# Performance work log

Measured on AMD Instinct MI355X. Metric: run time of the kernel, lower is better.

Reference implementation:

```python
import jax, jax.numpy as jnp
import numpy as np

B, C, H, W = 2, 192, 128, 128
NUM_HEADS = 6
AMP = 1
NUM_OFFSETS = 9


def bilinear_sample(img, grid):
    # img: (C, H, W); grid: (Hn, Wn, 2) in [-1,1], align_corners=True, zeros padding
    Hh, Ww = img.shape[1], img.shape[2]
    x = (grid[..., 0] + 1.0) * 0.5 * (Ww - 1)
    y = (grid[..., 1] + 1.0) * 0.5 * (Hh - 1)
    x0 = jnp.floor(x)
    y0 = jnp.floor(y)
    x1 = x0 + 1.0
    y1 = y0 + 1.0
    wx1 = x - x0
    wy1 = y - y0

    def gather(yi, xi):
        valid = ((xi >= 0) & (xi <= Ww - 1) & (yi >= 0) & (yi <= Hh - 1)).astype(img.dtype)
        xc = jnp.clip(xi, 0, Ww - 1).astype(jnp.int32)
        yc = jnp.clip(yi, 0, Hh - 1).astype(jnp.int32)
        return img[:, yc, xc] * valid  # (C, Hn, Wn)

    return (gather(y0, x0) * ((1 - wy1) * (1 - wx1))
            + gather(y0, x1) * ((1 - wy1) * wx1)
            + gather(y1, x0) * (wy1 * (1 - wx1))
            + gather(y1, x1) * (wy1 * wx1))


def setup_inputs() -> dict:
    key = jax.random.key(0)
    ks = jax.random.split(key, 8)
    s = 0.02
    Ch = C // NUM_HEADS
    return {
        "x_q": jax.random.normal(ks[0], (B, C, H, W), jnp.float32),
        "x_kv": jax.random.normal(ks[1], (B, C, H, W), jnp.float32),
        "w_q": jax.random.normal(ks[2], (C, C), jnp.float32) * s,
        "w_kv": jax.random.normal(ks[3], (2 * C, C), jnp.float32) * s,
        "w_off1": jax.random.normal(ks[4], (C, 2 * C, 3, 3), jnp.float32) * s,
        "b_off1": jnp.zeros((C,), jnp.float32),
        "w_off2": jax.random.normal(ks[5], (2 * NUM_OFFSETS, C), jnp.float32) * s,
        "b_off2": jnp.zeros((2 * NUM_OFFSETS,), jnp.float32),
        "w_proj": jax.random.normal(ks[6], (C, C), jnp.float32) * s,
        "b_proj": jnp.zeros((C,), jnp.float32),
    }


def reference(x_q, x_kv, w_q, w_kv, w_off1, b_off1, w_off2, b_off2, w_proj, b_proj):
    Ch = C // NUM_HEADS
    scale = Ch ** (-0.5)

    # 1x1 conv projections as channel matmuls
    q = jnp.einsum('oc,bchw->bohw', w_q, x_q) * scale
    kv = jnp.einsum('oc,bchw->bohw', w_kv, x_kv)
    k, v = kv[:, :C], kv[:, C:]  # kv.reshape(B,2,Ch,nh,H,W) -> first C channels are k

    # offset predictor: 3x3 conv -> relu -> 1x1 conv
    off_in = jnp.concatenate([x_q, x_kv], axis=1)
    h1 = jax.lax.conv_general_dilated(off_in, w_off1, (1, 1), 'SAME',
                                      dimension_numbers=('NCHW', 'OIHW', 'NCHW'))
    h1 = jax.nn.relu(h1 + b_off1[None, :, None, None])
    off = jnp.einsum('oc,bchw->bohw', w_off2, h1) + b_off2[None, :, None, None]
    off = off.reshape(B, NUM_OFFSETS, 2, H, W).transpose(0, 1, 3, 4, 2)  # (B,9,H,W,2)
    gx = off[..., 0] / (W - 1) * 2.0 - 1.0
    gy = off[..., 1] / (H - 1) * 2.0 - 1.0
    grid = jnp.stack([gx, gy], axis=-1)  # (B,9,H,W,2)

    # deformable gather: sample full-channel k/v at each of 9 per-pixel offset grids
    sample = jax.vmap(jax.vmap(bilinear_sample, in_axes=(None, 0)), in_axes=(0, 0))
    k_s = sample(k, grid).reshape(B, NUM_OFFSETS, Ch, NUM_HEADS, H, W)
    v_s = sample(v, grid).reshape(B, NUM_OFFSETS, Ch, NUM_HEADS, H, W)

    q = q.reshape(B, Ch, NUM_HEADS, H, W)

    pad = [(0, 0), (0, 0), (0, 0), (0, 0), (AMP, AMP), (AMP, AMP)]
    k_p = jnp.pad(k_s, pad)
    v_p = jnp.pad(v_s, pad)

    win = 2 * AMP + 1
    logits = []
    for i in range(win):
        for j in range(win):
            idx = i * win + j
            kp = k_p[:, idx, :, :, i:i + H, j:j + W]  # (B,Ch,nh,H,W)
            logits.append(jnp.einsum('bchxy,bchxy->bhxy', q, kp))
    attn = jax.nn.softmax(jnp.stack(logits, axis=1), axis=1)  # (B,9,nh,H,W)

    out = jnp.zeros((B, Ch, NUM_HEADS, H, W), x_q.dtype)
    for i in range(win):
        for j in range(win):
            idx = i * win + j
            vp = v_p[:, idx, :, :, i:i + H, j:j + W]
            out = out + attn[:, idx, None] * vp

    out = out.reshape(B, C, H, W)  # channel layout = (Ch, nh), matching torch reshape
    return jnp.einsum('oc,bchw->bohw', w_proj, out) + b_proj[None, :, None, None]
```

## Files before the change

### kernel.cpp

```cpp
#include <hip/hip_runtime.h>
#include <math.h>

#define HW 16384
#define NB 2
#define NC 192

typedef __attribute__((ext_vector_type(8))) short bh8;
typedef __attribute__((ext_vector_type(4))) float f32x4;

__device__ inline ushort f2bf(float f) {
  union { float f; unsigned int u; } x; x.f = f;
  unsigned int r = x.u + 0x7fffu + ((x.u >> 16) & 1u);
  return (ushort)(r >> 16);
}
__device__ inline float bf2f(ushort u) {
  union { unsigned int i; float f; } x; x.i = ((unsigned int)u) << 16;
  return x.f;
}
__device__ inline float asf(unsigned int u) {
  union { unsigned int i; float f; } x; x.i = u; return x.f;
}
__device__ inline unsigned int cvtpk(float lo, float hi) {
  unsigned int r;
  asm("v_cvt_pk_bf16_f32 %0, %1, %2" : "=v"(r) : "v"(lo), "v"(hi));
  return r;
}
__device__ inline void gl16(const ushort* g, char* l) {
  __builtin_amdgcn_global_load_lds(
      (const __attribute__((address_space(1))) unsigned int*)g,
      (__attribute__((address_space(3))) unsigned int*)l, 16, 0, 0);
}

__global__ void k_wpack(const float* __restrict__ w1, ushort* __restrict__ wpack) {
  int i = blockIdx.x * 256 + threadIdx.x;
  int s = i / 6144;
  int rem = i - s * 6144;
  int o = rem >> 5, kk = rem & 31;
  int dy = s / 36, t2 = s - dy * 36;
  int icc = t2 / 3, dxi = t2 - icc * 3;
  int ic = icc * 32 + kk;
  wpack[i] = f2bf(w1[(size_t)o * 3456 + (size_t)ic * 9 + dy * 3 + dxi]);
}

__global__ void k_wgpack(const float* __restrict__ wq, const float* __restrict__ wkv,
                         const float* __restrict__ wp, float scale,
                         ushort* __restrict__ wg) {
  int i = blockIdx.x * 256 + threadIdx.x;
  int r = i / NC, c = i - r * NC;
  float v;
  if (r < 192) {
    int orow = (r & 31) * 6 + (r >> 5);
    v = wq[(size_t)orow * NC + c] * scale;
  } else if (r < 576) {
    int rp = r - 192;
    int t = rp >= 192 ? 1 : 0;
    int cc = rp - t * 192;
    int orow = t * 192 + (cc & 31) * 6 + (cc >> 5);
    v = wkv[(size_t)orow * NC + c];
  } else {
    int rp = r - 576;
    v = wp[(size_t)rp * NC + ((c & 31) * 6 + (c >> 5))];
  }
  wg[i] = f2bf(v);
}

__global__ void k_zero(uint4* __restrict__ p) {
  p[(size_t)blockIdx.x * 256 + threadIdx.x] = make_uint4(0u, 0u, 0u, 0u);
}

__global__ __launch_bounds__(256) void k_xpack(const float* __restrict__ xq,
                                               const float* __restrict__ xkv,
                                               ushort* __restrict__ xpp) {
  __shared__ float t[NC][65];
  const int tid = threadIdx.x;
  const size_t r0 = (size_t)blockIdx.x * 64;
  const int b = (int)(r0 >> 14);
  const int px0 = (int)(r0 & 16383);
  const int y = px0 >> 7, x0 = px0 & 127;
  const float* src = (blockIdx.y == 0 ? xq : xkv) + (size_t)b * NC * HW + px0;
#pragma unroll
  for (int it = 0; it < 12; ++it) {
    int i = it * 256 + tid;
    int c = i >> 4, q4 = i & 15;
    float4 v = *(const float4*)(src + (size_t)c * HW + q4 * 4);
    t[c][q4 * 4 + 0] = v.x; t[c][q4 * 4 + 1] = v.y;
    t[c][q4 * 4 + 2] = v.z; t[c][q4 * 4 + 3] = v.w;
  }
  __syncthreads();
  ushort* dst = xpp + ((size_t)(b * 130 + y + 1) * 132 + x0 + 1) * 384 +
                blockIdx.y * 192;
#pragma unroll
  for (int it = 0; it < 6; ++it) {
    int i = it * 256 + tid;
    int px = i / 24, ch = i - px * 24;
    ushort4 u0, u1;
    u0.x = f2bf(t[ch * 8 + 0][px]); u0.y = f2bf(t[ch * 8 + 1][px]);
    u0.z = f2bf(t[ch * 8 + 2][px]); u0.w = f2bf(t[ch * 8 + 3][px]);
    u1.x = f2bf(t[ch * 8 + 4][px]); u1.y = f2bf(t[ch * 8 + 5][px]);
    u1.z = f2bf(t[ch * 8 + 6][px]); u1.w = f2bf(t[ch * 8 + 7][px]);
    *(ushort4*)&dst[(size_t)px * 384 + ch * 8] = u0;
    *(ushort4*)&dst[(size_t)px * 384 + ch * 8 + 4] = u1;
  }
}

__device__ inline void stage64(ushort* lds, const ushort* src, int rowStride,
                               int tid) {
#pragma unroll
  for (int it = 0; it < 6; ++it) {
    int i = it * 256 + tid;
    int row = i / 24, c = i - row * 24;
    int pos = (c & 24) | ((c & 7) ^ (row & 7));
    uint4 v = *(const uint4*)(src + (size_t)row * rowStride + c * 8);
    *(uint4*)&lds[row * NC + pos * 8] = v;
  }
}
__device__ inline bh8 frag64(const ushort* lds, int row, int c) {
  int pos = (c & 24) | ((c & 7) ^ (row & 7));
  return *(const bh8*)&lds[row * NC + pos * 8];
}

__global__ __launch_bounds__(256) void k_gemm_mfma(
    const ushort* __restrict__ xpp, const ushort* __restrict__ wg,
    ushort* __restrict__ qb, ushort* __restrict__ kb, ushort* __restrict__ vb) {
  __shared__ __attribute__((aligned(16))) ushort xs[64 * NC];
  __shared__ __attribute__((aligned(16))) ushort ws2[64 * NC];
  const int tid = threadIdx.x;
  const size_t p0 = (size_t)blockIdx.x * 64;
  const int bb = (int)(p0 >> 14);
  const int yy = (int)((p0 >> 7) & 127);
  const int xx0 = (int)(p0 & 127);
  const int which = blockIdx.y;
  const int cOff = (which == 0) ? 0 : 192;
  const ushort* src = xpp + ((size_t)(bb * 130 + yy + 1) * 132 + xx0 + 1) * 384 + cOff;
  const ushort* wbase = wg + (size_t)(which * 192) * NC;
  ushort* dst = which == 0 ? qb : (which == 1 ? kb : vb);
  stage64(xs, src, 384, tid);
  const int lid = tid & 15, g = (tid >> 4) & 3, wv = tid >> 6;
  const int wo = (wv & 1) * 32, wp = (wv >> 1) * 32;
  for (int ot = 0; ot < 3; ++ot) {
    if (ot) __syncthreads();
    stage64(ws2, wbase + (size_t)(ot * 64) * NC, NC, tid);
    __syncthreads();
    f32x4 acc[2][2];
#pragma unroll
    for (int m = 0; m < 2; ++m)
#pragma unroll
      for (int n = 0; n < 2; ++n) acc[m][n] = (f32x4){0.f, 0.f, 0.f, 0.f};
#pragma unroll
    for (int k = 0; k < 6; ++k) {
      bh8 a0 = frag64(ws2, wo + lid, k * 4 + g);
      bh8 a1 = frag64(ws2, wo + 16 + lid, k * 4 + g);
      bh8 b0 = frag64(xs, wp + lid, k * 4 + g);
      bh8 b1 = frag64(xs, wp + 16 + lid, k * 4 + g);
      acc[0][0] = __builtin_amdgcn_mfma_f32_16x16x32_bf16(a0, b0, acc[0][0], 0, 0, 0);
      acc[0][1] = __builtin_amdgcn_mfma_f32_16x16x32_bf16(a0, b1, acc[0][1], 0, 0, 0);
      acc[1][0] = __builtin_amdgcn_mfma_f32_16x16x32_bf16(a1, b0, acc[1][0], 0, 0, 0);
      acc[1][1] = __builtin_amdgcn_mfma_f32_16x16x32_bf16(a1, b1, acc[1][1], 0, 0, 0);
    }
    const int od = ot * 64;
#pragma unroll
    for (int m = 0; m < 2; ++m)
#pragma unroll
      for (int n = 0; n < 2; ++n) {
        int orow = od + wo + m * 16 + g * 4;
        size_t px = p0 + wp + n * 16 + lid;
        ushort4 u;
        u.x = f2bf(acc[m][n][0]); u.y = f2bf(acc[m][n][1]);
        u.z = f2bf(acc[m][n][2]); u.w = f2bf(acc[m][n][3]);
        *(ushort4*)&dst[px * NC + orow] = u;
      }
  }
}

__global__ __launch_bounds__(256) void k_proj_mfma(
    const ushort* __restrict__ pre, const ushort* __restrict__ wg,
    const float* __restrict__ bp, float* __restrict__ out) {
  __shared__ __attribute__((aligned(16))) ushort xs[64 * NC];
  __shared__ __attribute__((aligned(16))) ushort ws2[64 * NC];
  const int tid = threadIdx.x;
  const size_t p0 = (size_t)blockIdx.x * 64;
  const int o0 = blockIdx.y * 64;
  stage64(xs, pre + p0 * NC, NC, tid);
  stage64(ws2, wg + (size_t)o0 * NC, NC, tid);
  __syncthreads();
  const int lid = tid & 15, g = (tid >> 4) & 3, wv = tid >> 6;
  const int wo = (wv & 1) * 32, wp = (wv >> 1) * 32;
  f32x4 acc[2][2];
#pragma unroll
  for (int m = 0; m < 2; ++m)
#pragma unroll
    for (int n = 0; n < 2; ++n) acc[m][n] = (f32x4){0.f, 0.f, 0.f, 0.f};
#pragma unroll
  for (int k = 0; k < 6; ++k) {
    bh8 a0 = frag64(ws2, wo + lid, k * 4 + g);
    bh8 a1 = frag64(ws2, wo + 16 + lid, k * 4 + g);
    bh8 b0 = frag64(xs, wp + lid, k * 4 + g);
    bh8 b1 = frag64(xs, wp + 16 + lid, k * 4 + g);
    acc[0][0] = __builtin_amdgcn_mfma_f32_16x16x32_bf16(a0, b0, acc[0][0], 0, 0, 0);
    acc[0][1] = __builtin_amdgcn_mfma_f32_16x16x32_bf16(a0, b1, acc[0][1], 0, 0, 0);
    acc[1][0] = __builtin_amdgcn_mfma_f32_16x16x32_bf16(a1, b0, acc[1][0], 0, 0, 0);
    acc[1][1] = __builtin_amdgcn_mfma_f32_16x16x32_bf16(a1, b1, acc[1][1], 0, 0, 0);
  }
#pragma unroll
  for (int m = 0; m < 2; ++m)
#pragma unroll
    for (int n = 0; n < 2; ++n) {
      int oc = o0 + wo + m * 16 + g * 4;
      size_t pxf = p0 + wp + n * 16 + lid;
      int b = (int)(pxf >> 14);
      int px = (int)(pxf & 16383);
#pragma unroll
      for (int j = 0; j < 4; ++j)
        out[((size_t)b * NC + oc + j) * HW + px] = acc[m][n][j] + bp[oc + j];
    }
}

#define CP0 0
#define CP1 8448
#define CW0 16896
#define CW1 35328
__global__ __launch_bounds__(256, 3) void k_conv_mfma(
    const ushort* __restrict__ xpp, const ushort* __restrict__ wpack,
    const float* __restrict__ b1, ushort* __restrict__ h1) {
  __shared__ __attribute__((aligned(16))) char smem[53760];
  const int tid = threadIdx.x;
  const int bi = blockIdx.x;
  const int b = bi >> 8;
  const int y = (bi >> 1) & 127;
  const int oh = bi & 1;
  const int lid = tid & 15;
  const int g = (tid >> 4) & 3;
  const int wv = tid >> 6;
  const int lane = tid & 63;
  const int og = wv & 1;
  const int pg = wv >> 1;
  f32x4 acc[3][4];
#pragma unroll
  for (int m = 0; m < 3; ++m)
#pragma unroll
    for (int n = 0; n < 4; ++n) acc[m][n] = (f32x4){0.f, 0.f, 0.f, 0.f};

  auto stageP = [&](int icc, int dy, int buf) {
    const size_t rowbase = (size_t)(b * 130 + y + dy) * 132 * 384 + icc * 32;
    char* dst0 = smem + (buf ? CP1 : CP0);
    for (int grp = wv; grp < 9; grp += 4) {
      int i = grp * 64 + lane;
      if (i < 528) {
        int slot = i >> 2, ch = i & 3;
        gl16(xpp + rowbase + (size_t)slot * 384 + ((ch ^ ((slot >> 1) & 3)) << 3),
             dst0 + grp * 1024);
      }
    }
  };
  auto stageW = [&](int icc, int dy, int buf) {
    const ushort* wsrc = wpack + (size_t)((dy * 12 + icc) * 3) * 6144 + oh * 96 * 32;
    char* dst0 = smem + (buf ? CW1 : CW0);
    for (int grp = wv; grp < 18; grp += 4) {
      int i = grp * 64 + lane;
      int dxi = i / 384;
      int rem = i - dxi * 384;
      int o = rem >> 2, q = rem & 3;
      gl16(wsrc + (size_t)dxi * 6144 + o * 32 + ((q ^ ((o >> 1) & 3)) << 3),
           dst0 + grp * 1024);
    }
  };

  stageP(0, 0, 0);
  stageW(0, 0, 0);
  __syncthreads();
  int cur = 0;
  for (int s = 0; s < 36; ++s) {
    if (s < 35) {
      const int ns = s + 1;
      const int nicc = ns / 3, ndy = ns - nicc * 3;
      stageP(nicc, ndy, cur ^ 1);
      stageW(nicc, ndy, cur ^ 1);
    }
    const char* Pb = smem + (cur ? CP1 : CP0);
    const char* Wb = smem + (cur ? CW1 : CW0);
#pragma unroll
    for (int dxi = 0; dxi < 3; ++dxi) {
      bh8 af[3];
#pragma unroll
      for (int m = 0; m < 3; ++m) {
        int o = og * 48 + m * 16 + lid;
        af[m] = *(const bh8*)(Wb + ((dxi * 96 + o) << 6) +
                              ((g ^ ((o >> 1) & 3)) << 4));
      }
#pragma unroll
      for (int n = 0; n < 4; ++n) {
        int slot = pg * 64 + n * 16 + lid + dxi;
        bh8 bf = *(const bh8*)(Pb + (slot << 6) + ((g ^ ((slot >> 1) & 3)) << 4));
#pragma unroll
        for (int m = 0; m < 3; ++m)
          acc[m][n] = __builtin_amdgcn_mfma_f32_16x16x32_bf16(
              af[m], bf, acc[m][n], 0, 0, 0);
      }
    }
    __syncthreads();
    cur ^= 1;
  }

  const size_t pxbase = (size_t)(b << 14) + y * 128 + pg * 64;
#pragma unroll
  for (int m = 0; m < 3; ++m) {
    const int ob = oh * 96 + og * 48 + m * 16 + g * 4;
    float4 bv = *(const float4*)(b1 + ob);
#pragma unroll
    for (int n = 0; n < 4; ++n) {
      size_t px = pxbase + n * 16 + lid;
      h1[(size_t)(ob + 0) * (NB * HW) + px] = f2bf(fmaxf(acc[m][n][0] + bv.x, 0.f));
      h1[(size_t)(ob + 1) * (NB * HW) + px] = f2bf(fmaxf(acc[m][n][1] + bv.y, 0.f));
      h1[(size_t)(ob + 2) * (NB * HW) + px] = f2bf(fmaxf(acc[m][n][2] + bv.z, 0.f));
      h1[(size_t)(ob + 3) * (NB * HW) + px] = f2bf(fmaxf(acc[m][n][3] + bv.w, 0.f));
    }
  }
}

__global__ __launch_bounds__(256) void k_offhead(
    const ushort* __restrict__ h1, const float* __restrict__ w2,
    const float* __restrict__ b2, float* __restrict__ off) {
  __shared__ float w2l[18 * NC];
  const int tid = threadIdx.x;
  for (int i = tid; i < 18 * NC; i += 256) w2l[i] = w2[i];
  __syncthreads();
  const int px = tid & 127;
  const int jh = tid >> 7;
  const size_t p = (size_t)blockIdx.x * 128 + px;
  float acc[9];
#pragma unroll
  for (int jj = 0; jj < 9; ++jj) acc[jj] = b2[jh * 9 + jj];
  for (int c = 0; c < NC; ++c) {
    float v = bf2f(h1[(size_t)c * (NB * HW) + p]);
#pragma unroll
    for (int jj = 0; jj < 9; ++jj) acc[jj] += w2l[(jh * 9 + jj) * NC + c] * v;
  }
#pragma unroll
  for (int jj = 0; jj < 9; ++jj) off[p * 18 + jh * 9 + jj] = acc[jj];
}

__global__ __launch_bounds__(192, 6) void k_attn(
    const ushort* __restrict__ q, const ushort* __restrict__ k,
    const ushort* __restrict__ v, const float* __restrict__ off,
    ushort* __restrict__ pre) {
  const int s = threadIdx.x;
  const int pix = s / 48;
  const int sub = s - pix * 48;
  const int p = blockIdx.x * 4 + pix;
  const int b = p >> 14;
  const int pp = p & 16383;
  const int y = pp >> 7, x = pp & 127;

  uint2 qu = *(const uint2*)(q + (size_t)p * NC + 4 * sub);
  const float q0 = asf(qu.x << 16), q1 = asf(qu.x & 0xffff0000u);
  const float q2 = asf(qu.y << 16), q3 = asf(qu.y & 0xffff0000u);
  const unsigned int cbase = (unsigned int)b * (HW * NC) + 4 * sub;
  const int obase = b * HW;

  float pl[9];
  unsigned int vp0[9], vp1[9];
#pragma unroll
  for (int idx = 0; idx < 9; ++idx) {
    const int yy = y + idx / 3 - 1, xx = x + idx % 3 - 1;
    const bool inb = (yy >= 0) && (yy < 128) && (xx >= 0) && (xx < 128);
    float sx = 0.f, sy = 0.f;
    if (inb) {
      const int sp = obase + yy * 128 + xx;
      sx = off[sp * 18 + idx * 2 + 0];
      sy = off[sp * 18 + idx * 2 + 1];
    }
    const float fx0 = floorf(sx), fy0 = floorf(sy);
    const float wx1 = sx - fx0, wy1 = sy - fy0;
    const float wx0 = 1.f - wx1, wy0 = 1.f - wy1;
    const float inbf = inb ? 1.f : 0.f;
    const float wxm0 = wx0 * ((fx0 >= 0.f && fx0 <= 127.f) ? inbf : 0.f);
    const float wxm1 = wx1 * ((fx0 >= -1.f && fx0 <= 126.f) ? inbf : 0.f);
    const float wym0 = wy0 * ((fy0 >= 0.f && fy0 <= 127.f) ? 1.f : 0.f);
    const float wym1 = wy1 * ((fy0 >= -1.f && fy0 <= 126.f) ? 1.f : 0.f);
    const int ix0 = (int)fminf(fmaxf(fx0, 0.f), 127.f);
    const int iy0 = (int)fminf(fmaxf(fy0, 0.f), 127.f);
    const int ix1 = (int)fminf(fmaxf(fx0 + 1.f, 0.f), 127.f);
    const int iy1 = (int)fminf(fmaxf(fy0 + 1.f, 0.f), 127.f);
    const float w00 = wym0 * wxm0, w01 = wym0 * wxm1;
    const float w10 = wym1 * wxm0, w11 = wym1 * wxm1;
    const unsigned int e00 = cbase + (unsigned int)(iy0 * 128 + ix0) * 192u;
    const unsigned int e01 = cbase + (unsigned int)(iy0 * 128 + ix1) * 192u;
    const unsigned int e10 = cbase + (unsigned int)(iy1 * 128 + ix0) * 192u;
    const unsigned int e11 = cbase + (unsigned int)(iy1 * 128 + ix1) * 192u;
    float ks0 = 0.f, ks1 = 0.f, ks2 = 0.f, ks3 = 0.f;
    float vs0 = 0.f, vs1 = 0.f, vs2 = 0.f, vs3 = 0.f;
#define CORNER(W, E)                                            \
  {                                                             \
    uint2 kk = *(const uint2*)(k + (E));                        \
    uint2 vv = *(const uint2*)(v + (E));                        \
    ks0 = fmaf((W), asf(kk.x << 16), ks0);                      \
    ks1 = fmaf((W), asf(kk.x & 0xffff0000u), ks1);              \
    ks2 = fmaf((W), asf(kk.y << 16), ks2);                      \
    ks3 = fmaf((W), asf(kk.y & 0xffff0000u), ks3);              \
    vs0 = fmaf((W), asf(vv.x << 16), vs0);                      \
    vs1 = fmaf((W), asf(vv.x & 0xffff0000u), vs1);              \
    vs2 = fmaf((W), asf(vv.y << 16), vs2);                      \
    vs3 = fmaf((W), asf(vv.y & 0xffff0000u), vs3);              \
  }
    CORNER(w00, e00)
    CORNER(w01, e01)
    CORNER(w10, e10)
    CORNER(w11, e11)
#undef CORNER
    float pd = q0 * ks0 + q1 * ks1 + q2 * ks2 + q3 * ks3;
    pd += __shfl_xor(pd, 1);
    pd += __shfl_xor(pd, 2);
    pd += __shfl_xor(pd, 4);
    pl[idx] = pd;
    vp0[idx] = cvtpk(vs0, vs1);
    vp1[idx] = cvtpk(vs2, vs3);
  }
  float mx = pl[0];
#pragma unroll
  for (int i = 1; i < 9; ++i) mx = fmaxf(mx, pl[i]);
  float sm = 0.f;
#pragma unroll
  for (int i = 0; i < 9; ++i) { pl[i] = __expf(pl[i] - mx); sm += pl[i]; }
  const float inv = __builtin_amdgcn_rcpf(sm);
  float o0 = 0.f, o1 = 0.f, o2 = 0.f, o3 = 0.f;
#pragma unroll
  for (int i = 0; i < 9; ++i) {
    const float a = pl[i] * inv;
    o0 = fmaf(a, asf(vp0[i] << 16), o0);
    o1 = fmaf(a, asf(vp0[i] & 0xffff0000u), o1);
    o2 = fmaf(a, asf(vp1[i] << 16), o2);
    o3 = fmaf(a, asf(vp1[i] & 0xffff0000u), o3);
  }
  ushort4 r;
  r.x = f2bf(o0); r.y = f2bf(o1); r.z = f2bf(o2); r.w = f2bf(o3);
  *(ushort4*)(pre + (size_t)p * NC + 4 * sub) = r;
}

extern "C" void kernel_launch(void* const* d_in, const int* in_sizes, int n_in,
                              void* d_out, int out_size, void* d_ws, size_t ws_size,
                              hipStream_t stream) {
  const float* x_q    = (const float*)d_in[0];
  const float* x_kv   = (const float*)d_in[1];
  const float* w_q    = (const float*)d_in[2];
  const float* w_kv   = (const float*)d_in[3];
  const float* w_off1 = (const float*)d_in[4];
  const float* b_off1 = (const float*)d_in[5];
  const float* w_off2 = (const float*)d_in[6];
  const float* b_off2 = (const float*)d_in[7];
  const float* w_proj = (const float*)d_in[8];
  const float* b_proj = (const float*)d_in[9];
  float* out = (float*)d_out;

  char* W = (char*)d_ws;
  const size_t SB = (size_t)NB * HW * NC * 2;
  ushort* qb   = (ushort*)W;
  ushort* kb   = (ushort*)(W + SB);
  ushort* vb   = (ushort*)(W + 2 * SB);
  ushort* preb = (ushort*)(W + 3 * SB);
  ushort* h1b  = preb;
  ushort* wg   = (ushort*)(W + 4 * SB);
  ushort* xpp  = (ushort*)(W + 4 * SB + 294912);
  float*  offb = (float*)xpp;
  ushort* wpk  = (ushort*)d_out;

  const float scale = 0.17677669529663687f;
  dim3 blk(256);
  k_wpack<<<dim3(2592), blk, 0, stream>>>(w_off1, wpk);
  k_wgpack<<<dim3(576), blk, 0, stream>>>(w_q, w_kv, w_proj, scale, wg);
  k_zero<<<dim3(6435), blk, 0, stream>>>((uint4*)xpp);
  k_xpack<<<dim3(512, 2), blk, 0, stream>>>(x_q, x_kv, xpp);
  k_gemm_mfma<<<dim3(512, 3), blk, 0, stream>>>(xpp, wg, qb, kb, vb);
  k_conv_mfma<<<dim3(512), blk, 0, stream>>>(xpp, wpk, b_off1, h1b);
  k_offhead<<<dim3(NB * 128), blk, 0, stream>>>(h1b, w_off2, b_off2, offb);
  k_attn<<<dim3(8192), dim3(192), 0, stream>>>(qb, kb, vb, offb, preb);
  k_proj_mfma<<<dim3(512, 3), blk, 0, stream>>>(preb, wg + 576 * NC, b_proj, out);
}
```

Before: 190.1 us.

## Zero only padded halo of input buffer and share bilinear setup via LDS

The full-buffer zeroing kernel is replaced by one that writes only the halo rows and columns of the padded input buffer. To keep that halo intact, the offset buffer moves to its own workspace region instead of aliasing the padded input. In the attention kernel, the per-offset bilinear weights and corner indices are computed once per pixel by 9 lanes and shared through LDS, rather than recomputed redundantly by all 48 lanes. This removes a large memset and repeated ALU and offset loads, at the cost of a block barrier and extra LDS traffic.

```diff
diff --git a/kernel.cpp b/kernel.cpp
--- a/kernel.cpp
+++ b/kernel.cpp
@@ -64,8 +64,18 @@
   wg[i] = f2bf(v);
 }
 
-__global__ void k_zero(uint4* __restrict__ p) {
-  p[(size_t)blockIdx.x * 256 + threadIdx.x] = make_uint4(0u, 0u, 0u, 0u);
+__global__ void k_zerohalo(ushort* __restrict__ xpp) {
+  int i = blockIdx.x * 256 + threadIdx.x;
+  int t = i / 48;
+  int c = i - t * 48;
+  int b = t / 520;
+  int slot = t - b * 520;
+  int row, px;
+  if (slot < 132) { row = 0; px = slot; }
+  else if (slot < 264) { row = 129; px = slot - 132; }
+  else { int j = slot - 264; row = 1 + (j >> 1); px = (j & 1) ? 131 : 0; }
+  *(uint4*)(xpp + ((size_t)(b * 130 + row) * 132 + px) * 384 + c * 8) =
+      make_uint4(0u, 0u, 0u, 0u);
 }
 
 __global__ __launch_bounds__(256) void k_xpack(const float* __restrict__ xq,
@@ -343,6 +353,7 @@
     const ushort* __restrict__ q, const ushort* __restrict__ k,
     const ushort* __restrict__ v, const float* __restrict__ off,
     ushort* __restrict__ pre) {
+  __shared__ __attribute__((aligned(16))) float sw[4][9][8];
   const int s = threadIdx.x;
   const int pix = s / 48;
   const int sub = s - pix * 48;
@@ -351,21 +362,13 @@
   const int pp = p & 16383;
   const int y = pp >> 7, x = pp & 127;
 
-  uint2 qu = *(const uint2*)(q + (size_t)p * NC + 4 * sub);
-  const float q0 = asf(qu.x << 16), q1 = asf(qu.x & 0xffff0000u);
-  const float q2 = asf(qu.y << 16), q3 = asf(qu.y & 0xffff0000u);
-  const unsigned int cbase = (unsigned int)b * (HW * NC) + 4 * sub;
-  const int obase = b * HW;
-
-  float pl[9];
-  unsigned int vp0[9], vp1[9];
-#pragma unroll
-  for (int idx = 0; idx < 9; ++idx) {
+  if (sub < 9) {
+    const int idx = sub;
     const int yy = y + idx / 3 - 1, xx = x + idx % 3 - 1;
     const bool inb = (yy >= 0) && (yy < 128) && (xx >= 0) && (xx < 128);
     float sx = 0.f, sy = 0.f;
     if (inb) {
-      const int sp = obase + yy * 128 + xx;
+      const int sp = b * HW + yy * 128 + xx;
       sx = off[sp * 18 + idx * 2 + 0];
       sy = off[sp * 18 + idx * 2 + 1];
     }
@@ -381,18 +384,34 @@
     const int iy0 = (int)fminf(fmaxf(fy0, 0.f), 127.f);
     const int ix1 = (int)fminf(fmaxf(fx0 + 1.f, 0.f), 127.f);
     const int iy1 = (int)fminf(fmaxf(fy0 + 1.f, 0.f), 127.f);
-    const float w00 = wym0 * wxm0, w01 = wym0 * wxm1;
-    const float w10 = wym1 * wxm0, w11 = wym1 * wxm1;
-    const unsigned int e00 = cbase + (unsigned int)(iy0 * 128 + ix0) * 192u;
-    const unsigned int e01 = cbase + (unsigned int)(iy0 * 128 + ix1) * 192u;
-    const unsigned int e10 = cbase + (unsigned int)(iy1 * 128 + ix0) * 192u;
-    const unsigned int e11 = cbase + (unsigned int)(iy1 * 128 + ix1) * 192u;
+    float4 wv4 = make_float4(wym0 * wxm0, wym0 * wxm1, wym1 * wxm0, wym1 * wxm1);
+    uint4 ev4 = make_uint4((unsigned int)(iy0 * 128 + ix0) * 192u,
+                           (unsigned int)(iy0 * 128 + ix1) * 192u,
+                           (unsigned int)(iy1 * 128 + ix0) * 192u,
+                           (unsigned int)(iy1 * 128 + ix1) * 192u);
+    *(float4*)&sw[pix][idx][0] = wv4;
+    *(uint4*)&sw[pix][idx][4] = ev4;
+  }
+  __syncthreads();
+
+  uint2 qu = *(const uint2*)(q + (size_t)p * NC + 4 * sub);
+  const float q0 = asf(qu.x << 16), q1 = asf(qu.x & 0xffff0000u);
+  const float q2 = asf(qu.y << 16), q3 = asf(qu.y & 0xffff0000u);
+  const ushort* kl = k + (size_t)b * (HW * NC) + 4 * sub;
+  const ushort* vl = v + (size_t)b * (HW * NC) + 4 * sub;
+
+  float pl[9];
+  unsigned int vp0[9], vp1[9];
+#pragma unroll
+  for (int idx = 0; idx < 9; ++idx) {
+    const float4 w = *(const float4*)&sw[pix][idx][0];
+    const uint4 e = *(const uint4*)&sw[pix][idx][4];
     float ks0 = 0.f, ks1 = 0.f, ks2 = 0.f, ks3 = 0.f;
     float vs0 = 0.f, vs1 = 0.f, vs2 = 0.f, vs3 = 0.f;
 #define CORNER(W, E)                                            \
   {                                                             \
-    uint2 kk = *(const uint2*)(k + (E));                        \
-    uint2 vv = *(const uint2*)(v + (E));                        \
+    uint2 kk = *(const uint2*)(kl + (E));                       \
+    uint2 vv = *(const uint2*)(vl + (E));                       \
     ks0 = fmaf((W), asf(kk.x << 16), ks0);                      \
     ks1 = fmaf((W), asf(kk.x & 0xffff0000u), ks1);              \
     ks2 = fmaf((W), asf(kk.y << 16), ks2);                      \
@@ -402,10 +421,10 @@
     vs2 = fmaf((W), asf(vv.y << 16), vs2);                      \
     vs3 = fmaf((W), asf(vv.y & 0xffff0000u), vs3);              \
   }
-    CORNER(w00, e00)
-    CORNER(w01, e01)
-    CORNER(w10, e10)
-    CORNER(w11, e11)
+    CORNER(w.x, e.x)
+    CORNER(w.y, e.y)
+    CORNER(w.z, e.z)
+    CORNER(w.w, e.w)
 #undef CORNER
     float pd = q0 * ks0 + q1 * ks1 + q2 * ks2 + q3 * ks3;
     pd += __shfl_xor(pd, 1);
@@ -459,15 +478,15 @@
   ushort* preb = (ushort*)(W + 3 * SB);
   ushort* h1b  = preb;
   ushort* wg   = (ushort*)(W + 4 * SB);
-  ushort* xpp  = (ushort*)(W + 4 * SB + 294912);
-  float*  offb = (float*)xpp;
+  float*  offb = (float*)(W + 4 * SB + 294912);
+  ushort* xpp  = (ushort*)(W + 4 * SB + 294912 + 2359296);
   ushort* wpk  = (ushort*)d_out;
 
   const float scale = 0.17677669529663687f;
   dim3 blk(256);
   k_wpack<<<dim3(2592), blk, 0, stream>>>(w_off1, wpk);
   k_wgpack<<<dim3(576), blk, 0, stream>>>(w_q, w_kv, w_proj, scale, wg);
-  k_zero<<<dim3(6435), blk, 0, stream>>>((uint4*)xpp);
+  k_zerohalo<<<dim3(195), blk, 0, stream>>>(xpp);
   k_xpack<<<dim3(512, 2), blk, 0, stream>>>(x_q, x_kv, xpp);
   k_gemm_mfma<<<dim3(512, 3), blk, 0, stream>>>(xpp, wg, qb, kb, vb);
   k_conv_mfma<<<dim3(512), blk, 0, stream>>>(xpp, wpk, b_off1, h1b);
```

New measurement: 270.9 us. +42.5%, slower.
